# Performance work log

Measured on AMD Instinct MI355X. Metric: run time of the kernel, lower is better.

The kernel has to match this reference:

```python
import jax, jax.numpy as jnp
import numpy as np

N, E, D, O = 50000, 800000, 128, 128
BN_EPS = 1e-5

def setup_inputs() -> dict:
    key = jax.random.key(0)
    ks = jax.random.split(key, 12)
    s1 = 1.0 / np.sqrt(D)
    s2 = 1.0 / np.sqrt(O)
    return {
        "x": jax.random.normal(ks[0], (N, D), dtype=jnp.float32),
        "edge_index": jax.random.randint(ks[1], (2, E), 0, N, dtype=jnp.int64),
        "batch": jnp.zeros((N,), dtype=jnp.int64),
        "eps": jnp.float32(0.0),  # GINConv train_eps parameter, init 0
        "W1": jax.random.uniform(ks[2], (O, D), jnp.float32, -s1, s1),
        "b1": jax.random.uniform(ks[3], (O,), jnp.float32, -s1, s1),
        "gamma1": jnp.ones((O,), jnp.float32),
        "beta1": jnp.zeros((O,), jnp.float32),
        "W2": jax.random.uniform(ks[4], (O, O), jnp.float32, -s2, s2),
        "b2": jax.random.uniform(ks[5], (O,), jnp.float32, -s2, s2),
        "gamma2": jnp.ones((O,), jnp.float32),
        "beta2": jnp.zeros((O,), jnp.float32),
    }

def _bn(h, gamma, beta):
    # BatchNorm1d training mode: biased variance over nodes
    m = jnp.mean(h, axis=0)
    v = jnp.var(h, axis=0)
    return (h - m) * jax.lax.rsqrt(v + BN_EPS) * gamma + beta

def reference(x, edge_index, batch, eps, W1, b1, gamma1, beta1, W2, b2, gamma2, beta2):
    src, dst = edge_index[0], edge_index[1]
    # sum_{j in N(i)} x_j  (scatter-add over edges)
    agg = jax.ops.segment_sum(x[src], dst, num_segments=N)
    h = (1.0 + eps) * x + agg
    h = jax.nn.relu(_bn(h @ W1.T + b1, gamma1, beta1))
    h = jax.nn.relu(_bn(h @ W2.T + b2, gamma2, beta2))
    return h
```

## Files before the change

### kernel.cpp

```cpp
#include <hip/hip_runtime.h>
#include <hip/hip_bf16.h>

typedef __hip_bfloat16 bf16;
typedef unsigned short u16;
typedef unsigned int u32;
typedef __attribute__((ext_vector_type(8))) short short8;
typedef __attribute__((ext_vector_type(4))) float floatx4;

#define N_NODES 50000
#define N_EDGES 800000
#define DIM 128
#define NBUCK 391
#define CAP 2560
#define T_EDGES 8192

__device__ __forceinline__ u16 f2bfbits(float f) {
    bf16 h = __float2bfloat16(f);
    return *(u16*)&h;
}
__device__ __forceinline__ unsigned pack2(float a, float b) {
    return (unsigned)f2bfbits(a) | ((unsigned)f2bfbits(b) << 16);
}

__global__ void detect_kernel(const int* __restrict__ ei, int* __restrict__ flags,
                              int* __restrict__ gcur, float* __restrict__ stats) {
    int t = threadIdx.x;
    if (t < NBUCK) gcur[t] = 0;
    stats[t] = 0.f;
    if (t == 0) {
        int acc = 0;
        for (int k = 0; k < 64; k++) acc |= ei[2 * k + 1];
        flags[1] = (acc == 0) ? 1 : 0;
    }
}

__global__ void pack_kernel(const int* __restrict__ ei, const int* __restrict__ flags,
                            u32* __restrict__ packed) {
    int is64 = flags[1];
    int base = blockIdx.x * 1024 + threadIdx.x;
    #pragma unroll
    for (int j = 0; j < 4; j++) {
        int e = base + j * 256;
        if (e < N_EDGES) {
            int js = e, jd = N_EDGES + e;
            if (is64) { js = 2 * e; jd = 2 * (N_EDGES + e); }
            u32 s = (u32)ei[js], d = (u32)ei[jd];
            packed[e] = s | (d << 16);
        }
    }
}

__launch_bounds__(256)
__global__ void sort1_kernel(const u32* __restrict__ packed, u32* __restrict__ gbuck,
                             int* __restrict__ gcur) {
    __shared__ int hist[512];
    __shared__ int offs[512];
    __shared__ int partial[256];
    __shared__ int cur[NBUCK];
    __shared__ int gbase[NBUCK];
    __shared__ u32 buf[T_EDGES];
    int t = threadIdx.x;
    int e0 = blockIdx.x * T_EDGES;
    int n = N_EDGES - e0; if (n > T_EDGES) n = T_EDGES;

    for (int i = t; i < 512; i += 256) hist[i] = 0;
    for (int i = t; i < NBUCK; i += 256) cur[i] = 0;
    __syncthreads();

    u32 ed[T_EDGES / 256];
    #pragma unroll
    for (int j = 0; j < T_EDGES / 256; j++) {
        int idx = j * 256 + t;
        if (idx < n) {
            u32 p = packed[e0 + idx];
            ed[j] = p;
            atomicAdd(&hist[p >> 23], 1);
        }
    }
    __syncthreads();

    int a0 = hist[2 * t], a1 = hist[2 * t + 1];
    partial[t] = a0 + a1;
    __syncthreads();
    for (int d = 1; d < 256; d <<= 1) {
        int v = (t >= d) ? partial[t - d] : 0;
        __syncthreads();
        partial[t] += v;
        __syncthreads();
    }
    int ex = partial[t] - (a0 + a1);
    offs[2 * t] = ex; offs[2 * t + 1] = ex + a0;
    __syncthreads();

    #pragma unroll
    for (int j = 0; j < T_EDGES / 256; j++) {
        int idx = j * 256 + t;
        if (idx < n) {
            int b = ed[j] >> 23;
            int s = offs[b] + atomicAdd(&cur[b], 1);
            buf[s] = ed[j];
        }
    }
    for (int i = t; i < NBUCK; i += 256) {
        int c = hist[i];
        gbase[i] = c ? atomicAdd(&gcur[i], c) : 0;
    }
    __syncthreads();

    int wv = t >> 6, lane = t & 63;
    for (int b = wv; b < NBUCK; b += 4) {
        int c = hist[b], o = offs[b];
        long gb = (long)b * CAP + gbase[b];
        for (int j = lane; j < c; j += 64) gbuck[gb + j] = buf[o + j];
    }
}

__launch_bounds__(256)
__global__ void sort2_kernel(const u32* __restrict__ gbuck, const int* __restrict__ gcur,
                             u32* __restrict__ nbrs, int* __restrict__ starts,
                             int* __restrict__ counts) {
    __shared__ int cnt[128];
    __shared__ int offs[128];
    __shared__ int cur[128];
    __shared__ u32 buf[CAP];
    __shared__ u32 buf2[CAP];
    int b = blockIdx.x, t = threadIdx.x;
    int n = gcur[b];
    long base = (long)b * CAP;
    if (t < 128) { cnt[t] = 0; cur[t] = 0; }
    __syncthreads();

    for (int i = t; i < n; i += 256) {
        u32 p = gbuck[base + i];
        buf[i] = p;
        atomicAdd(&cnt[(p >> 16) & 127], 1);
    }
    __syncthreads();

    if (t < 128) offs[t] = cnt[t];
    __syncthreads();
    for (int d = 1; d < 128; d <<= 1) {
        int v = 0;
        if (t < 128 && t >= d) v = offs[t - d];
        __syncthreads();
        if (t < 128) offs[t] += v;
        __syncthreads();
    }
    if (t < 128) offs[t] -= cnt[t];
    __syncthreads();

    for (int i = t; i < n; i += 256) {
        u32 p = buf[i];
        int d = (p >> 16) & 127;
        int s = offs[d] + atomicAdd(&cur[d], 1);
        buf2[s] = p & 0xFFFF;
    }
    __syncthreads();

    for (int i = t; i < n; i += 256) nbrs[base + i] = buf2[i];
    if (t < 128) {
        starts[b * 128 + t] = (int)(base + offs[t]);
        counts[b * 128 + t] = cnt[t];
    }
}

__global__ void agg_kernel(const float2* __restrict__ xw, const int* __restrict__ starts,
                           const int* __restrict__ counts, const u32* __restrict__ nbrs,
                           const float* __restrict__ epsp, unsigned* __restrict__ hw) {
    int lane = threadIdx.x & 63;
    int node = blockIdx.x * 4 + (threadIdx.x >> 6);
    float ep1 = 1.0f + epsp[0];
    float2 self = xw[node * 64 + lane];
    float ax = ep1 * self.x, ay = ep1 * self.y;
    int s = starts[node], e = s + counts[node];
    int i = s;
    for (; i + 8 <= e; i += 8) {
        int n0 = nbrs[i],     n1 = nbrs[i + 1], n2 = nbrs[i + 2], n3 = nbrs[i + 3];
        int n4 = nbrs[i + 4], n5 = nbrs[i + 5], n6 = nbrs[i + 6], n7 = nbrs[i + 7];
        float2 u0 = xw[n0 * 64 + lane], u1 = xw[n1 * 64 + lane];
        float2 u2 = xw[n2 * 64 + lane], u3 = xw[n3 * 64 + lane];
        float2 u4 = xw[n4 * 64 + lane], u5 = xw[n5 * 64 + lane];
        float2 u6 = xw[n6 * 64 + lane], u7 = xw[n7 * 64 + lane];
        ax += ((u0.x + u1.x) + (u2.x + u3.x)) + ((u4.x + u5.x) + (u6.x + u7.x));
        ay += ((u0.y + u1.y) + (u2.y + u3.y)) + ((u4.y + u5.y) + (u6.y + u7.y));
    }
    for (; i + 2 <= e; i += 2) {
        int n0 = nbrs[i], n1 = nbrs[i + 1];
        float2 u0 = xw[n0 * 64 + lane], u1 = xw[n1 * 64 + lane];
        ax += u0.x + u1.x; ay += u0.y + u1.y;
    }
    if (i < e) {
        float2 u = xw[nbrs[i] * 64 + lane];
        ax += u.x; ay += u.y;
    }
    hw[node * 64 + lane] = pack2(ax, ay);
}

template<int TRANSFORM>
__launch_bounds__(256)
__global__ void gemm_mfma(const void* Ap, const float* __restrict__ Wp,
                          const float* __restrict__ bias,
                          const float* __restrict__ scale, const float* __restrict__ shift,
                          float* Yp, float* __restrict__ osum, float* __restrict__ osq) {
    __shared__ u16 sW[128 * 136];
    __shared__ float sScale[128], sShift[128], sBias[128], sSum[128], sSq[128];
    int t = threadIdx.x, lane = t & 63, wv = t >> 6;

    #pragma unroll
    for (int it = 0; it < 16; it++) {
        int q = it * 256 + t;
        int r = q >> 5, cq = q & 31;
        floatx4 w = ((const floatx4*)Wp)[q];
        u16 bb[4] = {f2bfbits(w[0]), f2bfbits(w[1]), f2bfbits(w[2]), f2bfbits(w[3])};
        *(uint2*)&sW[r * 136 + cq * 4] = *(uint2*)bb;
    }
    if (t < 128) {
        sSum[t] = 0.f; sSq[t] = 0.f; sBias[t] = bias[t];
        if (TRANSFORM) { sScale[t] = scale[t]; sShift[t] = shift[t]; }
    }
    __syncthreads();

    int tile = blockIdx.x * 4 + wv;
    if (tile < (N_NODES / 16)) {
        int col0 = lane & 15, quad = lane >> 4;
        int mrow = tile * 16 + col0;

        short8 afr[4];
        if (TRANSFORM == 0) {
            const u16* A = (const u16*)Ap;
            #pragma unroll
            for (int ks = 0; ks < 4; ks++)
                afr[ks] = *(const short8*)&A[mrow * DIM + ks * 32 + quad * 8];
        } else {
            const float* A = (const float*)Ap;
            #pragma unroll
            for (int ks = 0; ks < 4; ks++) {
                int kb = ks * 32 + quad * 8;
                floatx4 v0 = *(const floatx4*)&A[mrow * DIM + kb];
                floatx4 v1 = *(const floatx4*)&A[mrow * DIM + kb + 4];
                short8 r;
                #pragma unroll
                for (int j = 0; j < 4; j++) {
                    r[j]     = (short)f2bfbits(fmaxf(fmaf(v0[j], sScale[kb + j],     sShift[kb + j]),     0.f));
                    r[j + 4] = (short)f2bfbits(fmaxf(fmaf(v1[j], sScale[kb + 4 + j], sShift[kb + 4 + j]), 0.f));
                }
                afr[ks] = r;
            }
        }

        floatx4 acc[8];
        #pragma unroll
        for (int nt = 0; nt < 8; nt++) acc[nt] = (floatx4){0.f, 0.f, 0.f, 0.f};
        #pragma unroll
        for (int ks = 0; ks < 4; ks++) {
            #pragma unroll
            for (int nt = 0; nt < 8; nt++) {
                short8 bfr = *(const short8*)&sW[(nt * 16 + col0) * 136 + ks * 32 + quad * 8];
                acc[nt] = __builtin_amdgcn_mfma_f32_16x16x32_bf16(afr[ks], bfr, acc[nt], 0, 0, 0);
            }
        }

        #pragma unroll
        for (int nt = 0; nt < 8; nt++) {
            int col = nt * 16 + col0;
            float bb = sBias[col];
            float o0 = acc[nt][0] + bb, o1 = acc[nt][1] + bb;
            float o2 = acc[nt][2] + bb, o3 = acc[nt][3] + bb;
            int rbase = tile * 16 + quad * 4;
            Yp[(rbase + 0) * DIM + col] = o0;
            Yp[(rbase + 1) * DIM + col] = o1;
            Yp[(rbase + 2) * DIM + col] = o2;
            Yp[(rbase + 3) * DIM + col] = o3;
            float s = o0 + o1 + o2 + o3;
            float q = o0 * o0 + o1 * o1 + o2 * o2 + o3 * o3;
            s += __shfl_xor(s, 16); s += __shfl_xor(s, 32);
            q += __shfl_xor(q, 16); q += __shfl_xor(q, 32);
            if (quad == 0) { atomicAdd(&sSum[col], s); atomicAdd(&sSq[col], q); }
        }
    }
    __syncthreads();
    if (t < 128) { atomicAdd(&osum[t], sSum[t]); atomicAdd(&osq[t], sSq[t]); }
}

__global__ void finalize_kernel(const float* __restrict__ sum, const float* __restrict__ sumsq,
                                const float* __restrict__ gamma, const float* __restrict__ beta,
                                float* __restrict__ scale, float* __restrict__ shift) {
    int c = threadIdx.x;
    if (c < 128) {
        float m = sum[c] * (1.0f / N_NODES);
        float v = sumsq[c] * (1.0f / N_NODES) - m * m;
        v = fmaxf(v, 0.0f);
        float rs = rsqrtf(v + 1e-5f);
        float sc = gamma[c] * rs;
        scale[c] = sc;
        shift[c] = beta[c] - m * sc;
    }
}

__global__ void output_kernel(const float* __restrict__ Y, const float* __restrict__ scale,
                              const float* __restrict__ shift, float* __restrict__ out) {
    int i = (blockIdx.x * blockDim.x + threadIdx.x) * 8;
    if (i >= N_NODES * DIM) return;
    int c = i & 127;
    floatx4 v0 = *(const floatx4*)&Y[i];
    floatx4 v1 = *(const floatx4*)&Y[i + 4];
    floatx4 o0, o1;
    #pragma unroll
    for (int j = 0; j < 4; j++) {
        o0[j] = fmaxf(fmaf(v0[j], scale[c + j],     shift[c + j]),     0.f);
        o1[j] = fmaxf(fmaf(v1[j], scale[c + 4 + j], shift[c + 4 + j]), 0.f);
    }
    *(floatx4*)&out[i] = o0;
    *(floatx4*)&out[i + 4] = o1;
}

extern "C" void kernel_launch(void* const* d_in, const int* in_sizes, int n_in,
                              void* d_out, int out_size, void* d_ws, size_t ws_size,
                              hipStream_t stream) {
    const float* x   = (const float*)d_in[0];
    const int* eraw  = (const int*)d_in[1];
    const float* eps = (const float*)d_in[3];
    const float* W1  = (const float*)d_in[4];
    const float* b1  = (const float*)d_in[5];
    const float* g1  = (const float*)d_in[6];
    const float* be1 = (const float*)d_in[7];
    const float* W2  = (const float*)d_in[8];
    const float* b2  = (const float*)d_in[9];
    const float* g2  = (const float*)d_in[10];
    const float* be2 = (const float*)d_in[11];

    char* ws = (char*)d_ws;
    size_t off = 0;
    unsigned* h = (unsigned*)(ws + off); off += (size_t)N_NODES * DIM * 2;
    float* y = (float*)(ws + off);       off += (size_t)N_NODES * DIM * 4;
    float* stats = (float*)(ws + off);   off += 4 * 128 * 4;
    float* sum1 = stats, *sq1 = stats + 128, *sum2 = stats + 256, *sq2 = stats + 384;
    float* scale1 = (float*)(ws + off);  off += 128 * 4;
    float* shift1 = (float*)(ws + off);  off += 128 * 4;
    float* scale2 = (float*)(ws + off);  off += 128 * 4;
    float* shift2 = (float*)(ws + off);  off += 128 * 4;
    u32* packed = (u32*)(ws + off);      off += (size_t)N_EDGES * 4;
    u32* gbuck = (u32*)(ws + off);       off += (size_t)NBUCK * CAP * 4;
    u32* nbrs = (u32*)(ws + off);        off += (size_t)NBUCK * CAP * 4;
    int* starts = (int*)(ws + off);      off += (size_t)NBUCK * 128 * 4;
    int* counts = (int*)(ws + off);      off += (size_t)NBUCK * 128 * 4;
    int* gcur = (int*)(ws + off);        off += 512 * 4;
    int* flags = (int*)(ws + off);       off += 16 * 4;

    detect_kernel<<<1, 512, 0, stream>>>(eraw, flags, gcur, stats);
    pack_kernel<<<(N_EDGES + 1023) / 1024, 256, 0, stream>>>(eraw, flags, packed);
    sort1_kernel<<<(N_EDGES + T_EDGES - 1) / T_EDGES, 256, 0, stream>>>(packed, gbuck, gcur);
    sort2_kernel<<<NBUCK, 256, 0, stream>>>(gbuck, gcur, nbrs, starts, counts);
    agg_kernel<<<N_NODES / 4, 256, 0, stream>>>((const float2*)x, starts, counts, nbrs, eps, h);

    const int gemmGrid = (N_NODES / 16 + 3) / 4;
    gemm_mfma<0><<<gemmGrid, 256, 0, stream>>>(h, W1, b1, nullptr, nullptr, y, sum1, sq1);
    finalize_kernel<<<1, 128, 0, stream>>>(sum1, sq1, g1, be1, scale1, shift1);
    gemm_mfma<1><<<gemmGrid, 256, 0, stream>>>(y, W2, b2, scale1, shift1, y, sum2, sq2);
    finalize_kernel<<<1, 128, 0, stream>>>(sum2, sq2, g2, be2, scale2, shift2);
    output_kernel<<<(N_NODES * DIM / 8 + 255) / 256, 256, 0, stream>>>(y, scale2, shift2, (float*)d_out);
}
```

Baseline: 262.4 us.

## Store node features and intermediates in bf16, fuse edge packing into sort

```diff
diff --git a/kernel.cpp b/kernel.cpp
--- a/kernel.cpp
+++ b/kernel.cpp
@@ -21,6 +21,9 @@
 __device__ __forceinline__ unsigned pack2(float a, float b) {
     return (unsigned)f2bfbits(a) | ((unsigned)f2bfbits(b) << 16);
 }
+__device__ __forceinline__ float lo2f(u32 u) { u32 v = u << 16; return __builtin_bit_cast(float, v); }
+__device__ __forceinline__ float hi2f(u32 u) { u32 v = u & 0xFFFF0000u; return __builtin_bit_cast(float, v); }
+__device__ __forceinline__ float b162f(u16 u) { u32 v = (u32)u << 16; return __builtin_bit_cast(float, v); }
 
 __global__ void detect_kernel(const int* __restrict__ ei, int* __restrict__ flags,
                               int* __restrict__ gcur, float* __restrict__ stats) {
@@ -34,25 +37,19 @@
     }
 }
 
-__global__ void pack_kernel(const int* __restrict__ ei, const int* __restrict__ flags,
-                            u32* __restrict__ packed) {
-    int is64 = flags[1];
-    int base = blockIdx.x * 1024 + threadIdx.x;
-    #pragma unroll
-    for (int j = 0; j < 4; j++) {
-        int e = base + j * 256;
-        if (e < N_EDGES) {
-            int js = e, jd = N_EDGES + e;
-            if (is64) { js = 2 * e; jd = 2 * (N_EDGES + e); }
-            u32 s = (u32)ei[js], d = (u32)ei[jd];
-            packed[e] = s | (d << 16);
-        }
-    }
+__global__ void convert_x(const float* __restrict__ x, u32* __restrict__ xb) {
+    int i = (blockIdx.x * 256 + threadIdx.x) * 8;
+    floatx4 v0 = *(const floatx4*)&x[i];
+    floatx4 v1 = *(const floatx4*)&x[i + 4];
+    uint4 r;
+    r.x = pack2(v0[0], v0[1]); r.y = pack2(v0[2], v0[3]);
+    r.z = pack2(v1[0], v1[1]); r.w = pack2(v1[2], v1[3]);
+    *(uint4*)&xb[i / 2] = r;
 }
 
 __launch_bounds__(256)
-__global__ void sort1_kernel(const u32* __restrict__ packed, u32* __restrict__ gbuck,
-                             int* __restrict__ gcur) {
+__global__ void sort1_kernel(const int* __restrict__ ei, const int* __restrict__ flags,
+                             u32* __restrict__ gbuck, int* __restrict__ gcur) {
     __shared__ int hist[512];
     __shared__ int offs[512];
     __shared__ int partial[256];
@@ -60,6 +57,7 @@
     __shared__ int gbase[NBUCK];
     __shared__ u32 buf[T_EDGES];
     int t = threadIdx.x;
+    int is64 = flags[1];
     int e0 = blockIdx.x * T_EDGES;
     int n = N_EDGES - e0; if (n > T_EDGES) n = T_EDGES;
 
@@ -72,7 +70,10 @@
     for (int j = 0; j < T_EDGES / 256; j++) {
         int idx = j * 256 + t;
         if (idx < n) {
-            u32 p = packed[e0 + idx];
+            int e = e0 + idx;
+            int js = e, jd = N_EDGES + e;
+            if (is64) { js = 2 * e; jd = 2 * (N_EDGES + e); }
+            u32 p = (u32)ei[js] | ((u32)ei[jd] << 16);
             ed[j] = p;
             atomicAdd(&hist[p >> 23], 1);
         }
@@ -164,44 +165,45 @@
     }
 }
 
-__global__ void agg_kernel(const float2* __restrict__ xw, const int* __restrict__ starts,
+__global__ void agg_kernel(const u32* __restrict__ xb, const int* __restrict__ starts,
                            const int* __restrict__ counts, const u32* __restrict__ nbrs,
-                           const float* __restrict__ epsp, unsigned* __restrict__ hw) {
+                           const float* __restrict__ epsp, u32* __restrict__ hw) {
     int lane = threadIdx.x & 63;
     int node = blockIdx.x * 4 + (threadIdx.x >> 6);
     float ep1 = 1.0f + epsp[0];
-    float2 self = xw[node * 64 + lane];
-    float ax = ep1 * self.x, ay = ep1 * self.y;
+    u32 self = xb[node * 64 + lane];
+    float ax = ep1 * lo2f(self), ay = ep1 * hi2f(self);
     int s = starts[node], e = s + counts[node];
     int i = s;
     for (; i + 8 <= e; i += 8) {
         int n0 = nbrs[i],     n1 = nbrs[i + 1], n2 = nbrs[i + 2], n3 = nbrs[i + 3];
         int n4 = nbrs[i + 4], n5 = nbrs[i + 5], n6 = nbrs[i + 6], n7 = nbrs[i + 7];
-        float2 u0 = xw[n0 * 64 + lane], u1 = xw[n1 * 64 + lane];
-        float2 u2 = xw[n2 * 64 + lane], u3 = xw[n3 * 64 + lane];
-        float2 u4 = xw[n4 * 64 + lane], u5 = xw[n5 * 64 + lane];
-        float2 u6 = xw[n6 * 64 + lane], u7 = xw[n7 * 64 + lane];
-        ax += ((u0.x + u1.x) + (u2.x + u3.x)) + ((u4.x + u5.x) + (u6.x + u7.x));
-        ay += ((u0.y + u1.y) + (u2.y + u3.y)) + ((u4.y + u5.y) + (u6.y + u7.y));
+        u32 u0 = xb[n0 * 64 + lane], u1 = xb[n1 * 64 + lane];
+        u32 u2 = xb[n2 * 64 + lane], u3 = xb[n3 * 64 + lane];
+        u32 u4 = xb[n4 * 64 + lane], u5 = xb[n5 * 64 + lane];
+        u32 u6 = xb[n6 * 64 + lane], u7 = xb[n7 * 64 + lane];
+        ax += ((lo2f(u0) + lo2f(u1)) + (lo2f(u2) + lo2f(u3))) +
+              ((lo2f(u4) + lo2f(u5)) + (lo2f(u6) + lo2f(u7)));
+        ay += ((hi2f(u0) + hi2f(u1)) + (hi2f(u2) + hi2f(u3))) +
+              ((hi2f(u4) + hi2f(u5)) + (hi2f(u6) + hi2f(u7)));
     }
     for (; i + 2 <= e; i += 2) {
-        int n0 = nbrs[i], n1 = nbrs[i + 1];
-        float2 u0 = xw[n0 * 64 + lane], u1 = xw[n1 * 64 + lane];
-        ax += u0.x + u1.x; ay += u0.y + u1.y;
+        u32 u0 = xb[nbrs[i] * 64 + lane], u1 = xb[nbrs[i + 1] * 64 + lane];
+        ax += lo2f(u0) + lo2f(u1); ay += hi2f(u0) + hi2f(u1);
     }
     if (i < e) {
-        float2 u = xw[nbrs[i] * 64 + lane];
-        ax += u.x; ay += u.y;
+        u32 u = xb[nbrs[i] * 64 + lane];
+        ax += lo2f(u); ay += hi2f(u);
     }
     hw[node * 64 + lane] = pack2(ax, ay);
 }
 
 template<int TRANSFORM>
 __launch_bounds__(256)
-__global__ void gemm_mfma(const void* Ap, const float* __restrict__ Wp,
+__global__ void gemm_mfma(const u16* __restrict__ Ap, const float* __restrict__ Wp,
                           const float* __restrict__ bias,
                           const float* __restrict__ scale, const float* __restrict__ shift,
-                          float* Yp, float* __restrict__ osum, float* __restrict__ osq) {
+                          u16* __restrict__ Yp, float* __restrict__ osum, float* __restrict__ osq) {
     __shared__ u16 sW[128 * 136];
     __shared__ float sScale[128], sShift[128], sBias[128], sSum[128], sSq[128];
     int t = threadIdx.x, lane = t & 63, wv = t >> 6;
@@ -226,25 +228,20 @@
         int mrow = tile * 16 + col0;
 
         short8 afr[4];
-        if (TRANSFORM == 0) {
-            const u16* A = (const u16*)Ap;
-            #pragma unroll
-            for (int ks = 0; ks < 4; ks++)
-                afr[ks] = *(const short8*)&A[mrow * DIM + ks * 32 + quad * 8];
-        } else {
-            const float* A = (const float*)Ap;
-            #pragma unroll
-            for (int ks = 0; ks < 4; ks++) {
-                int kb = ks * 32 + quad * 8;
-                floatx4 v0 = *(const floatx4*)&A[mrow * DIM + kb];
-                floatx4 v1 = *(const floatx4*)&A[mrow * DIM + kb + 4];
+        #pragma unroll
+        for (int ks = 0; ks < 4; ks++) {
+            int kb = ks * 32 + quad * 8;
+            short8 a = *(const short8*)&Ap[mrow * DIM + kb];
+            if (TRANSFORM) {
                 short8 r;
                 #pragma unroll
-                for (int j = 0; j < 4; j++) {
-                    r[j]     = (short)f2bfbits(fmaxf(fmaf(v0[j], sScale[kb + j],     sShift[kb + j]),     0.f));
-                    r[j + 4] = (short)f2bfbits(fmaxf(fmaf(v1[j], sScale[kb + 4 + j], sShift[kb + 4 + j]), 0.f));
+                for (int j = 0; j < 8; j++) {
+                    float f = b162f((u16)a[j]);
+                    r[j] = (short)f2bfbits(fmaxf(fmaf(f, sScale[kb + j], sShift[kb + j]), 0.f));
                 }
                 afr[ks] = r;
+            } else {
+                afr[ks] = a;
             }
         }
 
@@ -267,10 +264,10 @@
             float o0 = acc[nt][0] + bb, o1 = acc[nt][1] + bb;
             float o2 = acc[nt][2] + bb, o3 = acc[nt][3] + bb;
             int rbase = tile * 16 + quad * 4;
-            Yp[(rbase + 0) * DIM + col] = o0;
-            Yp[(rbase + 1) * DIM + col] = o1;
-            Yp[(rbase + 2) * DIM + col] = o2;
-            Yp[(rbase + 3) * DIM + col] = o3;
+            Yp[(rbase + 0) * DIM + col] = f2bfbits(o0);
+            Yp[(rbase + 1) * DIM + col] = f2bfbits(o1);
+            Yp[(rbase + 2) * DIM + col] = f2bfbits(o2);
+            Yp[(rbase + 3) * DIM + col] = f2bfbits(o3);
             float s = o0 + o1 + o2 + o3;
             float q = o0 * o0 + o1 * o1 + o2 * o2 + o3 * o3;
             s += __shfl_xor(s, 16); s += __shfl_xor(s, 32);
@@ -297,18 +294,21 @@
     }
 }
 
-__global__ void output_kernel(const float* __restrict__ Y, const float* __restrict__ scale,
+__global__ void output_kernel(const u32* __restrict__ Y, const float* __restrict__ scale,
                               const float* __restrict__ shift, float* __restrict__ out) {
-    int i = (blockIdx.x * blockDim.x + threadIdx.x) * 8;
+    int i = (blockIdx.x * 256 + threadIdx.x) * 8;
     if (i >= N_NODES * DIM) return;
     int c = i & 127;
-    floatx4 v0 = *(const floatx4*)&Y[i];
-    floatx4 v1 = *(const floatx4*)&Y[i + 4];
+    uint4 v = *(const uint4*)&Y[i / 2];
+    u32 w[4] = {v.x, v.y, v.z, v.w};
     floatx4 o0, o1;
     #pragma unroll
     for (int j = 0; j < 4; j++) {
-        o0[j] = fmaxf(fmaf(v0[j], scale[c + j],     shift[c + j]),     0.f);
-        o1[j] = fmaxf(fmaf(v1[j], scale[c + 4 + j], shift[c + 4 + j]), 0.f);
+        float lo = lo2f(w[j]), hi = hi2f(w[j]);
+        float r0 = fmaxf(fmaf(lo, scale[c + 2 * j],     shift[c + 2 * j]),     0.f);
+        float r1 = fmaxf(fmaf(hi, scale[c + 2 * j + 1], shift[c + 2 * j + 1]), 0.f);
+        if (j < 2) { o0[2 * j] = r0; o0[2 * j + 1] = r1; }
+        else       { o1[2 * (j - 2)] = r0; o1[2 * (j - 2) + 1] = r1; }
     }
     *(floatx4*)&out[i] = o0;
     *(floatx4*)&out[i + 4] = o1;
@@ -331,15 +331,16 @@
 
     char* ws = (char*)d_ws;
     size_t off = 0;
-    unsigned* h = (unsigned*)(ws + off); off += (size_t)N_NODES * DIM * 2;
-    float* y = (float*)(ws + off);       off += (size_t)N_NODES * DIM * 4;
+    u32* xb = (u32*)(ws + off);          off += (size_t)N_NODES * DIM * 2;
+    u32* h1 = (u32*)(ws + off);          off += (size_t)N_NODES * DIM * 2;
+    u16* y1 = (u16*)(ws + off);          off += (size_t)N_NODES * DIM * 2;
+    u16* y2 = (u16*)(ws + off);          off += (size_t)N_NODES * DIM * 2;
     float* stats = (float*)(ws + off);   off += 4 * 128 * 4;
     float* sum1 = stats, *sq1 = stats + 128, *sum2 = stats + 256, *sq2 = stats + 384;
     float* scale1 = (float*)(ws + off);  off += 128 * 4;
     float* shift1 = (float*)(ws + off);  off += 128 * 4;
     float* scale2 = (float*)(ws + off);  off += 128 * 4;
     float* shift2 = (float*)(ws + off);  off += 128 * 4;
-    u32* packed = (u32*)(ws + off);      off += (size_t)N_EDGES * 4;
     u32* gbuck = (u32*)(ws + off);       off += (size_t)NBUCK * CAP * 4;
     u32* nbrs = (u32*)(ws + off);        off += (size_t)NBUCK * CAP * 4;
     int* starts = (int*)(ws + off);      off += (size_t)NBUCK * 128 * 4;
@@ -348,15 +349,15 @@
     int* flags = (int*)(ws + off);       off += 16 * 4;
 
     detect_kernel<<<1, 512, 0, stream>>>(eraw, flags, gcur, stats);
-    pack_kernel<<<(N_EDGES + 1023) / 1024, 256, 0, stream>>>(eraw, flags, packed);
-    sort1_kernel<<<(N_EDGES + T_EDGES - 1) / T_EDGES, 256, 0, stream>>>(packed, gbuck, gcur);
+    convert_x<<<N_NODES * DIM / (8 * 256), 256, 0, stream>>>(x, xb);
+    sort1_kernel<<<(N_EDGES + T_EDGES - 1) / T_EDGES, 256, 0, stream>>>(eraw, flags, gbuck, gcur);
     sort2_kernel<<<NBUCK, 256, 0, stream>>>(gbuck, gcur, nbrs, starts, counts);
-    agg_kernel<<<N_NODES / 4, 256, 0, stream>>>((const float2*)x, starts, counts, nbrs, eps, h);
+    agg_kernel<<<N_NODES / 4, 256, 0, stream>>>(xb, starts, counts, nbrs, eps, h1);
 
     const int gemmGrid = (N_NODES / 16 + 3) / 4;
-    gemm_mfma<0><<<gemmGrid, 256, 0, stream>>>(h, W1, b1, nullptr, nullptr, y, sum1, sq1);
+    gemm_mfma<0><<<gemmGrid, 256, 0, stream>>>((const u16*)h1, W1, b1, nullptr, nullptr, y1, sum1, sq1);
     finalize_kernel<<<1, 128, 0, stream>>>(sum1, sq1, g1, be1, scale1, shift1);
-    gemm_mfma<1><<<gemmGrid, 256, 0, stream>>>(y, W2, b2, scale1, shift1, y, sum2, sq2);
+    gemm_mfma<1><<<gemmGrid, 256, 0, stream>>>(y1, W2, b2, scale1, shift1, y2, sum2, sq2);
     finalize_kernel<<<1, 128, 0, stream>>>(sum2, sq2, g2, be2, scale2, shift2);
-    output_kernel<<<(N_NODES * DIM / 8 + 255) / 256, 256, 0, stream>>>(y, scale2, shift2, (float*)d_out);
-}
+    output_kernel<<<N_NODES * DIM / (8 * 256), 256, 0, stream>>>((const u32*)y2, scale2, shift2, (float*)d_out);
+}
```

New measurement: 240.6 us. 1.09x faster.
